# Performance work log

Measured on AMD Instinct MI355X. Metric: run time of the kernel, lower is better.

## Reference

```python
import jax, jax.numpy as jnp
import numpy as np
import math

D = 512      # input_size == hidden_size
TAU = 4      # length of att/spatial lists
N = 16384    # tokens (batch*H*W)

def setup_inputs() -> dict:
    key = jax.random.key(0)
    ks = jax.random.split(key, 16)
    s = 1.0 / math.sqrt(D)
    return {
        "T_t": jax.random.normal(ks[0], (N, D), jnp.float32),
        "S_t": jax.random.normal(ks[1], (N, D), jnp.float32),
        "t_att": jax.random.normal(ks[2], (TAU, N, D), jnp.float32),
        "s_att": jax.random.normal(ks[3], (TAU, N, D), jnp.float32),
        "t_spatial": jax.random.normal(ks[4], (TAU, N, D), jnp.float32),
        "s_spatial": jax.random.normal(ks[5], (TAU, N, D), jnp.float32),
        # fl_t: Linear(D, 3D); fl_t_next: Linear(D, D); same for s
        "W_t": jax.random.uniform(ks[6], (3 * D, D), jnp.float32, -s, s),
        "b_t": jax.random.uniform(ks[7], (3 * D,), jnp.float32, -s, s),
        "W_tn": jax.random.uniform(ks[8], (D, D), jnp.float32, -s, s),
        "b_tn": jax.random.uniform(ks[9], (D,), jnp.float32, -s, s),
        "W_s": jax.random.uniform(ks[10], (3 * D, D), jnp.float32, -s, s),
        "b_s": jax.random.uniform(ks[11], (3 * D,), jnp.float32, -s, s),
        "W_sn": jax.random.uniform(ks[12], (D, D), jnp.float32, -s, s),
        "b_sn": jax.random.uniform(ks[13], (D,), jnp.float32, -s, s),
    }

def reference(T_t, S_t, t_att, s_att, t_spatial, s_spatial,
              W_t, b_t, W_tn, b_tn, W_s, b_s, W_sn, b_sn):
    d = T_t.shape[-1]
    scale = 1.0 / jnp.sqrt(jnp.asarray(d, T_t.dtype))
    s_next = S_t @ W_sn.T + b_sn          # [N, D]
    t_next = T_t @ W_tn.T + b_tn          # [N, D]

    # trend weights: dot-product along feature dim, softmax over tau axis
    w_s = jax.nn.softmax(jnp.einsum('knd,nd->kn', s_att, s_next) * scale, axis=0)
    w_t = jax.nn.softmax(jnp.einsum('knd,nd->kn', t_spatial, t_next) * scale, axis=0)
    T_trend = jnp.einsum('knd,kn->nd', t_att, w_s)      # [N, D]
    S_trend = jnp.einsum('knd,kn->nd', s_spatial, w_t)  # [N, D]

    t_gate = jax.nn.sigmoid(t_next)
    s_gate = jax.nn.sigmoid(s_next)
    T_fusion = T_t * t_gate + (1.0 - t_gate) * T_trend
    S_fusion = S_t * s_gate + (1.0 - s_gate) * S_trend

    T_concat = T_fusion @ W_t.T + b_t     # [N, 3D]
    S_concat = S_fusion @ W_s.T + b_s
    t_g, t_t, t_s = jnp.split(T_concat, 3, axis=1)
    s_g, s_t, s_s = jnp.split(S_concat, 3, axis=1)
    T_gate = jax.nn.sigmoid(t_g)
    S_gate = jax.nn.sigmoid(s_g)
    T_new = T_gate * t_t + (1.0 - T_gate) * s_t
    S_new = S_gate * s_s + (1.0 - S_gate) * t_s
    return T_new, S_new
```

## Files before the change

kernel.cpp:

```cpp
#include <hip/hip_runtime.h>

#define NTOK 16384
#define DIM 512
#define NTAU 4

typedef __attribute__((ext_vector_type(4))) float f32x4;
typedef __attribute__((ext_vector_type(8))) short bf16x8;
typedef __attribute__((ext_vector_type(4))) unsigned short u16x4;
typedef __attribute__((ext_vector_type(8))) unsigned short u16x8;
typedef unsigned int u32;

__device__ inline unsigned short f2bf(float f) {
    union { float f; unsigned int u; } v; v.f = f;
    unsigned int u = v.u + 0x7FFFu + ((v.u >> 16) & 1u);
    return (unsigned short)(u >> 16);
}

__device__ inline void bf8_to_f32(u16x8 h, f32x4& a, f32x4& b) {
    union { unsigned int u; float f; } t;
#pragma unroll
    for (int e = 0; e < 4; e++) { t.u = ((unsigned int)h[e]) << 16; a[e] = t.f; }
#pragma unroll
    for (int e = 0; e < 4; e++) { t.u = ((unsigned int)h[4 + e]) << 16; b[e] = t.f; }
}

#define NTLOAD4(p) __builtin_nontemporal_load((const f32x4*)(p))

__device__ __forceinline__ void gload16(const void* g, void* l) {
    __builtin_amdgcn_global_load_lds((const __attribute__((address_space(1))) u32*)g,
                                     (__attribute__((address_space(3))) u32*)l, 16, 0, 0);
}

__global__ void convert_all(const float* __restrict__ a, const float* __restrict__ b,
                            const float* __restrict__ c, const float* __restrict__ d,
                            unsigned short* __restrict__ oa, unsigned short* __restrict__ ob,
                            unsigned short* __restrict__ oc, unsigned short* __restrict__ od) {
    int i = blockIdx.x * 256 + threadIdx.x;
    const float* s; unsigned short* t; int off;
    if (i < 65536)       { s = a; t = oa; off = i; }
    else if (i < 131072) { s = b; t = ob; off = i - 65536; }
    else if (i < 327680) { s = c; t = oc; off = i - 131072; }
    else                 { s = d; t = od; off = i - 327680; }
    f32x4 v = ((const f32x4*)s)[off];
    u16x4 o;
    o[0] = f2bf(v[0]); o[1] = f2bf(v[1]); o[2] = f2bf(v[2]); o[3] = f2bf(v[3]);
    ((u16x4*)t)[off] = o;
}

__global__ __launch_bounds__(256, 2) void gemm_next(
    const float* __restrict__ A, const unsigned short* __restrict__ W,
    const float* __restrict__ bias, unsigned short* __restrict__ out)
{
    __shared__ unsigned short lA[128][40];
    __shared__ unsigned short lB[128][40];
    const int tid = threadIdx.x;
    const int id = blockIdx.x + 4 * blockIdx.y;
    const int xcd = id & 7;
    const int idx = id >> 3;
    const int m0 = (xcd * 16 + (idx >> 2)) * 128;
    const int n0 = (idx & 3) * 128;
    const int lane = tid & 63;
    const int w = tid >> 6;
    const int wr = w >> 1, wc = w & 1;

    f32x4 acc[4][4];
#pragma unroll
    for (int i = 0; i < 4; i++)
#pragma unroll
        for (int j = 0; j < 4; j++) acc[i][j] = (f32x4){0.f, 0.f, 0.f, 0.f};

    const int arow = tid >> 3;
    const int acol = (tid & 7) * 4;
    const int brow = tid >> 2;
    const int bcol = (tid & 3) * 8;

    for (int k0 = 0; k0 < DIM; k0 += 32) {
#pragma unroll
        for (int i = 0; i < 4; i++) {
            int r = arow + 32 * i;
            f32x4 v = *(const f32x4*)(A + (size_t)(m0 + r) * DIM + k0 + acol);
            u16x4 o;
            o[0] = f2bf(v[0]); o[1] = f2bf(v[1]); o[2] = f2bf(v[2]); o[3] = f2bf(v[3]);
            *(u16x4*)&lA[r][acol] = o;
        }
#pragma unroll
        for (int i = 0; i < 2; i++) {
            int r = brow + 64 * i;
            u16x8 v = *(const u16x8*)(W + (size_t)(n0 + r) * DIM + k0 + bcol);
            *(u16x8*)&lB[r][bcol] = v;
        }
        __syncthreads();

        bf16x8 af[4], bfr[4];
#pragma unroll
        for (int i = 0; i < 4; i++)
            af[i] = *(const bf16x8*)&lA[wr * 64 + i * 16 + (lane & 15)][(lane >> 4) * 8];
#pragma unroll
        for (int j = 0; j < 4; j++)
            bfr[j] = *(const bf16x8*)&lB[wc * 64 + j * 16 + (lane & 15)][(lane >> 4) * 8];
#pragma unroll
        for (int i = 0; i < 4; i++)
#pragma unroll
            for (int j = 0; j < 4; j++)
                acc[i][j] = __builtin_amdgcn_mfma_f32_16x16x32_bf16(af[i], bfr[j], acc[i][j], 0, 0, 0);
        __syncthreads();
    }

#pragma unroll
    for (int j = 0; j < 4; j++) {
        int n = n0 + wc * 64 + j * 16 + (lane & 15);
        float bv = bias[n];
#pragma unroll
        for (int i = 0; i < 4; i++) {
            int mbase = m0 + wr * 64 + i * 16 + (lane >> 4) * 4;
#pragma unroll
            for (int r = 0; r < 4; r++)
                out[(size_t)(mbase + r) * DIM + n] = f2bf(acc[i][j][r] + bv);
        }
    }
}

__global__ __launch_bounds__(256) void dots_kernel(
    const float* __restrict__ s_att, const float* __restrict__ t_spatial,
    const unsigned short* __restrict__ t_next, const unsigned short* __restrict__ s_next,
    float* __restrict__ w_all)
{
    const int lane = threadIdx.x & 63;
    const int n = (blockIdx.x << 2) + (threadIdx.x >> 6);
    const int c = lane * 8;
    const size_t rb = (size_t)n * DIM + c;
    const float scale = 0.04419417382415922f;

    f32x4 tn_a, tn_b, sn_a, sn_b;
    bf8_to_f32(*(const u16x8*)(t_next + rb), tn_a, tn_b);
    bf8_to_f32(*(const u16x8*)(s_next + rb), sn_a, sn_b);

    float dws[NTAU], dwt[NTAU];
#pragma unroll
    for (int k = 0; k < NTAU; k++) {
        const size_t kb = ((size_t)k * NTOK + n) * DIM + c;
        f32x4 a0 = NTLOAD4(s_att + kb);
        f32x4 a1 = NTLOAD4(s_att + kb + 4);
        f32x4 b0 = NTLOAD4(t_spatial + kb);
        f32x4 b1 = NTLOAD4(t_spatial + kb + 4);
        dws[k] = a0[0]*sn_a[0]+a0[1]*sn_a[1]+a0[2]*sn_a[2]+a0[3]*sn_a[3]
               + a1[0]*sn_b[0]+a1[1]*sn_b[1]+a1[2]*sn_b[2]+a1[3]*sn_b[3];
        dwt[k] = b0[0]*tn_a[0]+b0[1]*tn_a[1]+b0[2]*tn_a[2]+b0[3]*tn_a[3]
               + b1[0]*tn_b[0]+b1[1]*tn_b[1]+b1[2]*tn_b[2]+b1[3]*tn_b[3];
    }
#pragma unroll
    for (int k = 0; k < NTAU; k++) {
        float v = dws[k];
#pragma unroll
        for (int off = 32; off; off >>= 1) v += __shfl_xor(v, off);
        dws[k] = v * scale;
        float u = dwt[k];
#pragma unroll
        for (int off = 32; off; off >>= 1) u += __shfl_xor(u, off);
        dwt[k] = u * scale;
    }

    float ms = fmaxf(fmaxf(dws[0], dws[1]), fmaxf(dws[2], dws[3]));
    float mt = fmaxf(fmaxf(dwt[0], dwt[1]), fmaxf(dwt[2], dwt[3]));
    f32x4 wsv, wtv;
    float ssum = 0.f, tsum = 0.f;
#pragma unroll
    for (int k = 0; k < NTAU; k++) {
        wsv[k] = __expf(dws[k] - ms); ssum += wsv[k];
        wtv[k] = __expf(dwt[k] - mt); tsum += wtv[k];
    }
    float rs = 1.f / ssum, rt = 1.f / tsum;
#pragma unroll
    for (int k = 0; k < NTAU; k++) { wsv[k] *= rs; wtv[k] *= rt; }

    if (lane == 0) {
        *(f32x4*)(w_all + (size_t)n * 8)     = wsv;
        *(f32x4*)(w_all + (size_t)n * 8 + 4) = wtv;
    }
}

__global__ __launch_bounds__(256) void fusion_kernel(
    const float* __restrict__ T_t, const float* __restrict__ S_t,
    const float* __restrict__ t_att, const float* __restrict__ s_spatial,
    const unsigned short* __restrict__ t_next, const unsigned short* __restrict__ s_next,
    const float* __restrict__ w_all,
    unsigned short* __restrict__ Tf, unsigned short* __restrict__ Sf)
{
    const int lane = threadIdx.x & 63;
    const int n = (blockIdx.x << 2) + (threadIdx.x >> 6);
    const int c = lane * 8;
    const size_t rb = (size_t)n * DIM + c;

    f32x4 wsv = *(const f32x4*)(w_all + (size_t)n * 8);
    f32x4 wtv = *(const f32x4*)(w_all + (size_t)n * 8 + 4);

    f32x4 Tta = {0,0,0,0}, Ttb = {0,0,0,0}, Sta = {0,0,0,0}, Stb = {0,0,0,0};
#pragma unroll
    for (int k = 0; k < NTAU; k++) {
        const size_t kb = ((size_t)k * NTOK + n) * DIM + c;
        f32x4 ta = NTLOAD4(t_att + kb);
        f32x4 tb = NTLOAD4(t_att + kb + 4);
        f32x4 sa = NTLOAD4(s_spatial + kb);
        f32x4 sb = NTLOAD4(s_spatial + kb + 4);
        float wk = wsv[k], vk = wtv[k];
#pragma unroll
        for (int e = 0; e < 4; e++) {
            Tta[e] += wk * ta[e]; Ttb[e] += wk * tb[e];
            Sta[e] += vk * sa[e]; Stb[e] += vk * sb[e];
        }
    }

    f32x4 tn_a, tn_b, sn_a, sn_b;
    bf8_to_f32(*(const u16x8*)(t_next + rb), tn_a, tn_b);
    bf8_to_f32(*(const u16x8*)(s_next + rb), sn_a, sn_b);
    f32x4 Ta = NTLOAD4(T_t + rb);
    f32x4 Tb = NTLOAD4(T_t + rb + 4);
    f32x4 Sa = NTLOAD4(S_t + rb);
    f32x4 Sb = NTLOAD4(S_t + rb + 4);

    u16x8 oT, oS;
#pragma unroll
    for (int e = 0; e < 4; e++) {
        float gt_a = 1.f / (1.f + __expf(-tn_a[e]));
        float gt_b = 1.f / (1.f + __expf(-tn_b[e]));
        float gs_a = 1.f / (1.f + __expf(-sn_a[e]));
        float gs_b = 1.f / (1.f + __expf(-sn_b[e]));
        oT[e]     = f2bf(Ta[e] * gt_a + (1.f - gt_a) * Tta[e]);
        oT[4 + e] = f2bf(Tb[e] * gt_b + (1.f - gt_b) * Ttb[e]);
        oS[e]     = f2bf(Sa[e] * gs_a + (1.f - gs_a) * Sta[e]);
        oS[4 + e] = f2bf(Sb[e] * gs_b + (1.f - gs_b) * Stb[e]);
    }
    *(u16x8*)(Tf + rb) = oT;
    *(u16x8*)(Sf + rb) = oS;
}

__global__ __launch_bounds__(256, 2) void gemm_final(
    const unsigned short* __restrict__ Tf, const unsigned short* __restrict__ Sf,
    const unsigned short* __restrict__ Wt, const unsigned short* __restrict__ Ws,
    const float* __restrict__ bt, const float* __restrict__ bs,
    float* __restrict__ out)
{
    __shared__ __align__(16) unsigned short lT[2][128][32];
    __shared__ __align__(16) unsigned short lS[2][128][32];
    __shared__ __align__(16) unsigned short lW[2][192][32];
    const int tid = threadIdx.x;
    const int id = blockIdx.x + 16 * blockIdx.y;
    const int xcd = id & 7;
    const int idx = id >> 3;
    const int m0 = (xcd * 16 + (idx >> 4)) * 128;
    const int j0 = (idx & 15) * 32;
    const int lane = tid & 63;
    const int w = tid >> 6, wr = w >> 1, wc = w & 1;

    f32x4 acc[6][4];
#pragma unroll
    for (int g = 0; g < 6; g++)
#pragma unroll
        for (int i = 0; i < 4; i++) acc[g][i] = (f32x4){0.f, 0.f, 0.f, 0.f};

    const int srow = lane >> 2;
    const int sg   = lane & 3;

    auto stage = [&](int buf, int kt) {
        const int k0 = kt * 32;
        if (w < 2) {
            const int rbs = w * 64;
#pragma unroll
            for (int i = 0; i < 4; i++) {
                const int row = rbs + i * 16 + srow;
                const int lg = sg ^ ((row >> 1) & 3);
                gload16(Tf + (size_t)(m0 + row) * DIM + k0 + lg * 8, &lT[buf][rbs + i * 16][0]);
                gload16(Sf + (size_t)(m0 + row) * DIM + k0 + lg * 8, &lS[buf][rbs + i * 16][0]);
            }
        } else {
            const int rbs = (w - 2) * 96;
#pragma unroll
            for (int i = 0; i < 6; i++) {
                const int r = rbs + i * 16 + srow;
                const int lg = sg ^ ((r >> 1) & 3);
                const int g = r >> 5;
                const unsigned short* src = (g < 3) ? Wt : Ws;
                const int wrow = (g < 3 ? g : g - 3) * DIM + j0 + (r & 31);
                gload16(src + (size_t)wrow * DIM + k0 + lg * 8, &lW[buf][rbs + i * 16][0]);
            }
        }
    };

    stage(0, 0);
    __syncthreads();

    int cur = 0;
    for (int kt = 0; kt < 16; ++kt) {
        if (kt < 15) stage(cur ^ 1, kt + 1);

        bf16x8 aT[4], aS[4];
#pragma unroll
        for (int i = 0; i < 4; i++) {
            const int row = wr * 64 + i * 16 + (lane & 15);
            const int pg = (lane >> 4) ^ ((row >> 1) & 3);
            aT[i] = *(const bf16x8*)&lT[cur][row][pg * 8];
            aS[i] = *(const bf16x8*)&lS[cur][row][pg * 8];
        }
#pragma unroll
        for (int g = 0; g < 6; g++) {
            const int r = g * 32 + wc * 16 + (lane & 15);
            const int pg = (lane >> 4) ^ ((r >> 1) & 3);
            bf16x8 bw = *(const bf16x8*)&lW[cur][r][pg * 8];
#pragma unroll
            for (int i = 0; i < 4; i++)
                acc[g][i] = __builtin_amdgcn_mfma_f32_16x16x32_bf16(
                    (g < 3) ? aT[i] : aS[i], bw, acc[g][i], 0, 0, 0);
        }
        __syncthreads();
        cur ^= 1;
    }

    const int j = j0 + wc * 16 + (lane & 15);
    const float btg = bt[j], btt = bt[512 + j], bts = bt[1024 + j];
    const float bsg = bs[j], bst = bs[512 + j], bss = bs[1024 + j];
#pragma unroll
    for (int i = 0; i < 4; i++) {
        int mbase = m0 + wr * 64 + i * 16 + (lane >> 4) * 4;
#pragma unroll
        for (int r = 0; r < 4; r++) {
            float TG = acc[0][i][r] + btg;
            float TT = acc[1][i][r] + btt;
            float TS = acc[2][i][r] + bts;
            float SG = acc[3][i][r] + bsg;
            float ST = acc[4][i][r] + bst;
            float SS = acc[5][i][r] + bss;
            float gT = 1.f / (1.f + __expf(-TG));
            float gS = 1.f / (1.f + __expf(-SG));
            size_t m = (size_t)(mbase + r);
            out[m * DIM + j] = gT * TT + (1.f - gT) * ST;
            out[(size_t)NTOK * DIM + m * DIM + j] = gS * SS + (1.f - gS) * TS;
        }
    }
}

extern "C" void kernel_launch(void* const* d_in, const int* in_sizes, int n_in,
                              void* d_out, int out_size, void* d_ws, size_t ws_size,
                              hipStream_t stream) {
    const float* T_t       = (const float*)d_in[0];
    const float* S_t       = (const float*)d_in[1];
    const float* t_att     = (const float*)d_in[2];
    const float* s_att     = (const float*)d_in[3];
    const float* t_spatial = (const float*)d_in[4];
    const float* s_spatial = (const float*)d_in[5];
    const float* W_t  = (const float*)d_in[6];
    const float* b_t  = (const float*)d_in[7];
    const float* W_tn = (const float*)d_in[8];
    const float* b_tn = (const float*)d_in[9];
    const float* W_s  = (const float*)d_in[10];
    const float* b_s  = (const float*)d_in[11];
    const float* W_sn = (const float*)d_in[12];
    const float* b_sn = (const float*)d_in[13];
    float* out = (float*)d_out;

    char* ws = (char*)d_ws;
    unsigned short* t_next = (unsigned short*)(ws + 0);
    unsigned short* s_next = (unsigned short*)(ws + 16777216);
    unsigned short* Tf     = (unsigned short*)(ws + 33554432);
    unsigned short* Sf     = (unsigned short*)(ws + 50331648);
    unsigned short* Wtn_b  = (unsigned short*)(ws + 67108864);
    unsigned short* Wsn_b  = (unsigned short*)(ws + 67633152);
    unsigned short* Wt_b   = (unsigned short*)(ws + 68157440);
    unsigned short* Ws_b   = (unsigned short*)(ws + 69730304);
    float*          w_all  = (float*)(ws + 71303168);

    convert_all<<<2048, 256, 0, stream>>>(W_tn, W_sn, W_t, W_s,
                                          Wtn_b, Wsn_b, Wt_b, Ws_b);

    dim3 g1(DIM / 128, NTOK / 128);
    gemm_next<<<g1, 256, 0, stream>>>(T_t, Wtn_b, b_tn, t_next);
    gemm_next<<<g1, 256, 0, stream>>>(S_t, Wsn_b, b_sn, s_next);

    dots_kernel<<<4096, 256, 0, stream>>>(s_att, t_spatial, t_next, s_next, w_all);

    fusion_kernel<<<4096, 256, 0, stream>>>(T_t, S_t, t_att, s_spatial,
                                            t_next, s_next, w_all, Tf, Sf);

    dim3 g3(DIM / 32, NTOK / 128);
    gemm_final<<<g3, 256, 0, stream>>>(Tf, Sf, Wt_b, Ws_b, b_t, b_s, out);
}
```

Measured before the change: 293.3 us.

## Widen final GEMM column tile to 64 and merge the two next-state GEMMs

The final GEMM now computes 64 output columns per block instead of 32, so each block holds twice the accumulators and reuses every loaded Tf/Sf tile across twice as many weight rows. This halves how often the activation tiles are reloaded, and weight staging is now shared across all four waves. Separately, the two next-state GEMM launches are merged into one 1024-block launch that chooses T or S from the block index, removing a launch and letting both halves share the GPU. The cost is doubled accumulator registers (192 floats per thread) and larger LDS use, which may reduce occupancy or cause spills.

```diff
diff --git a/kernel.cpp b/kernel.cpp
--- a/kernel.cpp
+++ b/kernel.cpp
@@ -47,16 +47,24 @@
     ((u16x4*)t)[off] = o;
 }
 
-__global__ __launch_bounds__(256, 2) void gemm_next(
-    const float* __restrict__ A, const unsigned short* __restrict__ W,
-    const float* __restrict__ bias, unsigned short* __restrict__ out)
+__global__ __launch_bounds__(256, 2) void gemm_next2(
+    const float* __restrict__ T_t, const float* __restrict__ S_t,
+    const unsigned short* __restrict__ Wtn, const unsigned short* __restrict__ Wsn,
+    const float* __restrict__ btn, const float* __restrict__ bsn,
+    unsigned short* __restrict__ t_next, unsigned short* __restrict__ s_next)
 {
     __shared__ unsigned short lA[128][40];
     __shared__ unsigned short lB[128][40];
     const int tid = threadIdx.x;
-    const int id = blockIdx.x + 4 * blockIdx.y;
+    const int id = blockIdx.x;
     const int xcd = id & 7;
-    const int idx = id >> 3;
+    const int rest = id >> 3;
+    const int mat = rest & 1;
+    const int idx = rest >> 1;
+    const float* A = mat ? S_t : T_t;
+    const unsigned short* W = mat ? Wsn : Wtn;
+    const float* bias = mat ? bsn : btn;
+    unsigned short* out = mat ? s_next : t_next;
     const int m0 = (xcd * 16 + (idx >> 2)) * 128;
     const int n0 = (idx & 3) * 128;
     const int lane = tid & 63;
@@ -242,25 +250,35 @@
 {
     __shared__ __align__(16) unsigned short lT[2][128][32];
     __shared__ __align__(16) unsigned short lS[2][128][32];
-    __shared__ __align__(16) unsigned short lW[2][192][32];
+    __shared__ __align__(16) unsigned short lW[2][384][32];
     const int tid = threadIdx.x;
-    const int id = blockIdx.x + 16 * blockIdx.y;
+    const int id = blockIdx.x + 8 * blockIdx.y;
     const int xcd = id & 7;
     const int idx = id >> 3;
-    const int m0 = (xcd * 16 + (idx >> 4)) * 128;
-    const int j0 = (idx & 15) * 32;
+    const int m0 = (xcd * 16 + (idx >> 3)) * 128;
+    const int j0 = (idx & 7) * 64;
     const int lane = tid & 63;
     const int w = tid >> 6, wr = w >> 1, wc = w & 1;
 
-    f32x4 acc[6][4];
+    f32x4 acc[6][4][2];
 #pragma unroll
     for (int g = 0; g < 6; g++)
 #pragma unroll
-        for (int i = 0; i < 4; i++) acc[g][i] = (f32x4){0.f, 0.f, 0.f, 0.f};
+        for (int i = 0; i < 4; i++)
+#pragma unroll
+            for (int jj = 0; jj < 2; jj++) acc[g][i][jj] = (f32x4){0.f, 0.f, 0.f, 0.f};
 
     const int srow = lane >> 2;
     const int sg   = lane & 3;
 
+    auto stageW = [&](int buf, int k0, int rbase) {
+        const int r = rbase + srow;
+        const int lg = sg ^ ((r >> 1) & 3);
+        const int g = r >> 6;
+        const unsigned short* src = (g < 3) ? Wt : Ws;
+        const int wrow = (g < 3 ? g : g - 3) * DIM + j0 + (r & 63);
+        gload16(src + (size_t)wrow * DIM + k0 + lg * 8, &lW[buf][rbase][0]);
+    };
     auto stage = [&](int buf, int kt) {
         const int k0 = kt * 32;
         if (w < 2) {
@@ -272,17 +290,13 @@
                 gload16(Tf + (size_t)(m0 + row) * DIM + k0 + lg * 8, &lT[buf][rbs + i * 16][0]);
                 gload16(Sf + (size_t)(m0 + row) * DIM + k0 + lg * 8, &lS[buf][rbs + i * 16][0]);
             }
+            stageW(buf, k0, w * 32);
+            stageW(buf, k0, w * 32 + 16);
         } else {
-            const int rbs = (w - 2) * 96;
-#pragma unroll
-            for (int i = 0; i < 6; i++) {
-                const int r = rbs + i * 16 + srow;
-                const int lg = sg ^ ((r >> 1) & 3);
-                const int g = r >> 5;
-                const unsigned short* src = (g < 3) ? Wt : Ws;
-                const int wrow = (g < 3 ? g : g - 3) * DIM + j0 + (r & 31);
-                gload16(src + (size_t)wrow * DIM + k0 + lg * 8, &lW[buf][rbs + i * 16][0]);
-            }
+            const int rbs = 64 + (w - 2) * 160;
+#pragma unroll
+            for (int i = 0; i < 10; i++)
+                stageW(buf, k0, rbs + i * 16);
         }
     };
 
@@ -303,37 +317,43 @@
         }
 #pragma unroll
         for (int g = 0; g < 6; g++) {
-            const int r = g * 32 + wc * 16 + (lane & 15);
-            const int pg = (lane >> 4) ^ ((r >> 1) & 3);
-            bf16x8 bw = *(const bf16x8*)&lW[cur][r][pg * 8];
-#pragma unroll
-            for (int i = 0; i < 4; i++)
-                acc[g][i] = __builtin_amdgcn_mfma_f32_16x16x32_bf16(
-                    (g < 3) ? aT[i] : aS[i], bw, acc[g][i], 0, 0, 0);
+#pragma unroll
+            for (int jj = 0; jj < 2; jj++) {
+                const int r = g * 64 + wc * 32 + jj * 16 + (lane & 15);
+                const int pg = (lane >> 4) ^ ((r >> 1) & 3);
+                bf16x8 bw = *(const bf16x8*)&lW[cur][r][pg * 8];
+#pragma unroll
+                for (int i = 0; i < 4; i++)
+                    acc[g][i][jj] = __builtin_amdgcn_mfma_f32_16x16x32_bf16(
+                        (g < 3) ? aT[i] : aS[i], bw, acc[g][i][jj], 0, 0, 0);
+            }
         }
         __syncthreads();
         cur ^= 1;
     }
 
-    const int j = j0 + wc * 16 + (lane & 15);
-    const float btg = bt[j], btt = bt[512 + j], bts = bt[1024 + j];
-    const float bsg = bs[j], bst = bs[512 + j], bss = bs[1024 + j];
-#pragma unroll
-    for (int i = 0; i < 4; i++) {
-        int mbase = m0 + wr * 64 + i * 16 + (lane >> 4) * 4;
-#pragma unroll
-        for (int r = 0; r < 4; r++) {
-            float TG = acc[0][i][r] + btg;
-            float TT = acc[1][i][r] + btt;
-            float TS = acc[2][i][r] + bts;
-            float SG = acc[3][i][r] + bsg;
-            float ST = acc[4][i][r] + bst;
-            float SS = acc[5][i][r] + bss;
-            float gT = 1.f / (1.f + __expf(-TG));
-            float gS = 1.f / (1.f + __expf(-SG));
-            size_t m = (size_t)(mbase + r);
-            out[m * DIM + j] = gT * TT + (1.f - gT) * ST;
-            out[(size_t)NTOK * DIM + m * DIM + j] = gS * SS + (1.f - gS) * TS;
+#pragma unroll
+    for (int jj = 0; jj < 2; jj++) {
+        const int j = j0 + wc * 32 + jj * 16 + (lane & 15);
+        const float btg = bt[j], btt = bt[512 + j], bts = bt[1024 + j];
+        const float bsg = bs[j], bst = bs[512 + j], bss = bs[1024 + j];
+#pragma unroll
+        for (int i = 0; i < 4; i++) {
+            int mbase = m0 + wr * 64 + i * 16 + (lane >> 4) * 4;
+#pragma unroll
+            for (int r = 0; r < 4; r++) {
+                float TG = acc[0][i][jj][r] + btg;
+                float TT = acc[1][i][jj][r] + btt;
+                float TS = acc[2][i][jj][r] + bts;
+                float SG = acc[3][i][jj][r] + bsg;
+                float ST = acc[4][i][jj][r] + bst;
+                float SS = acc[5][i][jj][r] + bss;
+                float gT = 1.f / (1.f + __expf(-TG));
+                float gS = 1.f / (1.f + __expf(-SG));
+                size_t m = (size_t)(mbase + r);
+                out[m * DIM + j] = gT * TT + (1.f - gT) * ST;
+                out[(size_t)NTOK * DIM + m * DIM + j] = gS * SS + (1.f - gS) * TS;
+            }
         }
     }
 }
@@ -371,15 +391,14 @@
     convert_all<<<2048, 256, 0, stream>>>(W_tn, W_sn, W_t, W_s,
                                           Wtn_b, Wsn_b, Wt_b, Ws_b);
 
-    dim3 g1(DIM / 128, NTOK / 128);
-    gemm_next<<<g1, 256, 0, stream>>>(T_t, Wtn_b, b_tn, t_next);
-    gemm_next<<<g1, 256, 0, stream>>>(S_t, Wsn_b, b_sn, s_next);
+    gemm_next2<<<1024, 256, 0, stream>>>(T_t, S_t, Wtn_b, Wsn_b, b_tn, b_sn,
+                                         t_next, s_next);
 
     dots_kernel<<<4096, 256, 0, stream>>>(s_att, t_spatial, t_next, s_next, w_all);
 
     fusion_kernel<<<4096, 256, 0, stream>>>(T_t, S_t, t_att, s_spatial,
                                             t_next, s_next, w_all, Tf, Sf);
 
-    dim3 g3(DIM / 32, NTOK / 128);
+    dim3 g3(8, 128);
     gemm_final<<<g3, 256, 0, stream>>>(Tf, Sf, Wt_b, Ws_b, b_t, b_s, out);
 }
```

Result: slower. 307.3 us (+4.8%).
